# Performance work log

Measured on AMD Instinct MI355X. Metric: run time of the kernel, lower is better.

The kernel has to match this reference:

```python
import jax, jax.numpy as jnp
import numpy as np

N_PER, B, D, CIN, COUT = 500000, 2, 192, 64, 64
EPS = 1e-5


def _build_coords_and_nbrs():
    rng = np.random.default_rng(0)
    cells, xs, ys, zs = [], [], [], []
    for b in range(B):
        cell = rng.choice(D ** 3, size=N_PER, replace=False).astype(np.int64)
        cells.append(cell + b * D ** 3)
        xs.append(cell // (D * D))
        ys.append((cell // D) % D)
        zs.append(cell % D)
    lin = np.concatenate(cells)
    x = np.concatenate(xs); y = np.concatenate(ys); z = np.concatenate(zs)
    N = lin.shape[0]
    order = np.argsort(lin)
    slin = lin[order]

    def nbrs(axis_stride, cvals):
        cols = []
        for d in (-1, 0, 1):
            tgt = lin + d * axis_stride
            valid = (cvals + d >= 0) & (cvals + d < D)
            pos = np.searchsorted(slin, tgt)
            pc = np.clip(pos, 0, N - 1)
            found = valid & (slin[pc] == tgt)
            cols.append(np.where(found, order[pc], -1))
        return np.stack(cols, axis=1).astype(np.int32)  # [N,3]

    return nbrs(1, z), nbrs(D, y), nbrs(D * D, x)


def setup_inputs() -> dict:
    key = jax.random.key(0)
    k1, k2, k3, k4 = jax.random.split(key, 4)
    nbr_z, nbr_y, nbr_x = _build_coords_and_nbrs()
    N = B * N_PER
    s = 1.0 / np.sqrt(3.0 * CIN)
    return {
        "feats": jax.random.normal(k1, (N, CIN), jnp.float32),
        "W1": jax.random.normal(k2, (3, CIN, CIN), jnp.float32) * s,
        "W2": jax.random.normal(k3, (3, CIN, CIN), jnp.float32) * s,
        "W3": jax.random.normal(k4, (3, CIN, COUT), jnp.float32) * s,
        "gamma": jnp.ones((COUT,), jnp.float32),
        "beta": jnp.zeros((COUT,), jnp.float32),
        "nbr_z": jnp.asarray(nbr_z),
        "nbr_y": jnp.asarray(nbr_y),
        "nbr_x": jnp.asarray(nbr_x),
    }


def _sparse_conv1d(feats, W, nbr):
    # feats [N,Cin], W [3,Cin,Cout], nbr [N,3] (-1 = missing neighbor)
    mask = (nbr >= 0)
    g = feats[jnp.where(mask, nbr, 0)]              # [N,3,Cin] gather
    g = g * mask[..., None].astype(feats.dtype)     # zero missing taps
    return jnp.einsum('nkc,kcd->nd', g, W)          # GEMM over taps


def reference(feats, W1, W2, W3, gamma, beta, nbr_z, nbr_y, nbr_x):
    h = _sparse_conv1d(feats, W1, nbr_z)   # conv (1,1,3)
    h = _sparse_conv1d(h, W2, nbr_y)       # conv (1,3,1)
    h = _sparse_conv1d(h, W3, nbr_x)       # conv (3,1,1)
    # BatchNorm over the N active points (training-mode batch stats)
    mean = jnp.mean(h, axis=0)
    var = jnp.var(h, axis=0)
    h = (h - mean) * (gamma / jnp.sqrt(var + EPS)) + beta
    return jax.nn.relu(h)
```

## Files before the change

### kernel.cpp

```cpp
#include <hip/hip_runtime.h>
#include <cstdint>
#include <cstddef>


typedef __attribute__((ext_vector_type(4))) float float4v;
typedef __attribute__((ext_vector_type(4))) unsigned int uint4v;
typedef __attribute__((ext_vector_type(8))) __bf16 bf16x8;
typedef __attribute__((ext_vector_type(8))) unsigned short ushort8;

__device__ __forceinline__ unsigned short f2bf_bits(float f) {
    unsigned int u = __builtin_bit_cast(unsigned int, f);
    u += 0x7fffu + ((u >> 16) & 1u);
    return (unsigned short)(u >> 16);
}
__device__ __forceinline__ float bf2f(unsigned short b) {
    unsigned int u = ((unsigned int)b) << 16;
    return __builtin_bit_cast(float, u);
}

__device__ __forceinline__ void gld_lds16(const void* g, void* l) {
    __builtin_amdgcn_global_load_lds(
        (const __attribute__((address_space(1))) unsigned int*)g,
        (__attribute__((address_space(3))) unsigned int*)l, 16, 0, 0);
}

__global__ __launch_bounds__(256)
void cvt_kernel(const float* __restrict__ in, unsigned short* __restrict__ out,
                size_t n8)
{
    size_t i = (size_t)blockIdx.x * 256 + threadIdx.x;
    const size_t stride = (size_t)gridDim.x * 256;
    for (; i < n8; i += stride) {
        const float4v* p = reinterpret_cast<const float4v*>(in + i * 8);
        float4v f0 = p[0], f1 = p[1];
        ushort8 u;
#pragma unroll
        for (int j = 0; j < 4; ++j) {
            u[j]     = f2bf_bits(f0[j]);
            u[j + 4] = f2bf_bits(f1[j]);
        }
        *reinterpret_cast<uint4v*>(out + i * 8) = __builtin_bit_cast(uint4v, u);
    }
}

template<bool DO_STATS>
__global__ __launch_bounds__(256, 3)
void conv_kernel(const unsigned short* __restrict__ Ain,
                 const float* __restrict__ Wg,
                 const int* __restrict__ nbr,
                 unsigned short* __restrict__ Hout,
                 const unsigned short* __restrict__ Zrow,
                 float* __restrict__ stats, int ntiles)
{
    __shared__ unsigned short Bld[192 * 64];
    __shared__ unsigned short Abuf[4][2][1024];
    __shared__ unsigned short Tld[4][16 * 72];
    __shared__ float ssum[64], ssq[64];

    const int tid = threadIdx.x;
    for (int i = tid; i < 192 * 64; i += 256) {
        int kc = i >> 6, d = i & 63;
        Bld[(((kc >> 3) << 6) + d) * 8 + (kc & 7)] = f2bf_bits(Wg[i]);
    }
    if (DO_STATS && tid < 64) { ssum[tid] = 0.f; ssq[tid] = 0.f; }
    __syncthreads();

    const int lane = tid & 63;
    const int wid  = tid >> 6;
    const int l15  = lane & 15;
    const int quad = lane >> 4;

    bf16x8 bfr[6][4];
#pragma unroll
    for (int s = 0; s < 6; ++s)
#pragma unroll
        for (int nt = 0; nt < 4; ++nt) {
            const uint4v* p = reinterpret_cast<const uint4v*>(
                &Bld[(((s * 4 + quad) << 6) + nt * 16 + l15) * 8]);
            bfr[s][nt] = __builtin_bit_cast(bf16x8, *p);
        }

    const int rl  = lane >> 3;
    const int seg = (lane & 7) ^ rl;
    const char* zaddr = (const char*)Zrow + seg * 16;
    const char* abase = (const char*)Ain;

    const int frb = ((l15 >> 3) << 10) + ((l15 & 7) << 7);
    const int fr0 = frb + ((quad ^ (l15 & 7)) << 4);
    const int fr1 = frb + (((quad + 4) ^ (l15 & 7)) << 4);

    char* buf0 = (char*)&Abuf[wid][0][0];
    char* buf1 = (char*)&Abuf[wid][1][0];

    float lsum[4] = {0.f, 0.f, 0.f, 0.f};
    float lsq[4]  = {0.f, 0.f, 0.f, 0.f};
    unsigned short* tl = Tld[wid];

    const int S = gridDim.x * 4;
    int t = blockIdx.x * 4 + wid;
    if (t < ntiles) {
        int idxc[6], idxn[6];
#pragma unroll
        for (int tap = 0; tap < 3; ++tap)
#pragma unroll
            for (int h = 0; h < 2; ++h)
                idxc[tap * 2 + h] = nbr[(size_t)(t * 16 + h * 8 + rl) * 3 + tap];
        {
            int i0 = idxc[0], i1 = idxc[1];
            const char* g0 = (i0 >= 0) ? abase + (((size_t)(unsigned)i0) << 7) + seg * 16 : zaddr;
            const char* g1 = (i1 >= 0) ? abase + (((size_t)(unsigned)i1) << 7) + seg * 16 : zaddr;
            gld_lds16(g0, buf0);
            gld_lds16(g1, buf0 + 1024);
        }
        int tn = t + S;
        if (tn < ntiles) {
#pragma unroll
            for (int tap = 0; tap < 3; ++tap)
#pragma unroll
                for (int h = 0; h < 2; ++h)
                    idxn[tap * 2 + h] = nbr[(size_t)(tn * 16 + h * 8 + rl) * 3 + tap];
        }
        int p = 0;
        while (true) {
            float4v acc[4] = {};
#pragma unroll
            for (int tap = 0; tap < 3; ++tap) {
                char* curb = p ? buf1 : buf0;
                char* nxtb = p ? buf0 : buf1;
                __asm__ volatile("s_waitcnt vmcnt(0)" ::: "memory");
                uint4v ua0 = *reinterpret_cast<const uint4v*>(curb + fr0);
                uint4v ua1 = *reinterpret_cast<const uint4v*>(curb + fr1);
                int nj0, nj1;
                bool have_next;
                if (tap < 2) {
                    nj0 = idxc[(tap + 1) * 2]; nj1 = idxc[(tap + 1) * 2 + 1];
                    have_next = true;
                } else {
                    nj0 = idxn[0]; nj1 = idxn[1];
                    have_next = (tn < ntiles);
                }
                if (have_next) {
                    const char* g0 = (nj0 >= 0) ? abase + (((size_t)(unsigned)nj0) << 7) + seg * 16 : zaddr;
                    const char* g1 = (nj1 >= 0) ? abase + (((size_t)(unsigned)nj1) << 7) + seg * 16 : zaddr;
                    gld_lds16(g0, nxtb);
                    gld_lds16(g1, nxtb + 1024);
                }
                bf16x8 a0 = __builtin_bit_cast(bf16x8, ua0);
                bf16x8 a1 = __builtin_bit_cast(bf16x8, ua1);
                const int s0 = tap * 2;
#pragma unroll
                for (int nt = 0; nt < 4; ++nt)
                    acc[nt] = __builtin_amdgcn_mfma_f32_16x16x32_bf16(a0, bfr[s0][nt], acc[nt], 0, 0, 0);
#pragma unroll
                for (int nt = 0; nt < 4; ++nt)
                    acc[nt] = __builtin_amdgcn_mfma_f32_16x16x32_bf16(a1, bfr[s0 + 1][nt], acc[nt], 0, 0, 0);
                p ^= 1;
            }

            if (DO_STATS) {
#pragma unroll
                for (int nt = 0; nt < 4; ++nt) {
                    lsum[nt] += acc[nt][0] + acc[nt][1] + acc[nt][2] + acc[nt][3];
                    lsq[nt]  += acc[nt][0] * acc[nt][0] + acc[nt][1] * acc[nt][1]
                              + acc[nt][2] * acc[nt][2] + acc[nt][3] * acc[nt][3];
                }
            }

#pragma unroll
            for (int nt = 0; nt < 4; ++nt)
#pragma unroll
                for (int r = 0; r < 4; ++r)
                    tl[(quad * 4 + r) * 72 + nt * 16 + l15] = f2bf_bits(acc[nt][r]);
            __asm__ volatile("s_waitcnt lgkmcnt(0)" ::: "memory");
            unsigned short* op = Hout + ((size_t)t << 10);
#pragma unroll
            for (int c = 0; c < 2; ++c) {
                int chunk = c * 64 + lane;
                int r = chunk >> 3;
                int off = (chunk & 7) * 8;
                uint4v v = *reinterpret_cast<const uint4v*>(&tl[r * 72 + off]);
                *reinterpret_cast<uint4v*>(op + (r << 6) + off) = v;
            }
            __asm__ volatile("s_waitcnt lgkmcnt(0)" ::: "memory");

            t = tn; tn += S;
            if (t >= ntiles) break;
#pragma unroll
            for (int j = 0; j < 6; ++j) idxc[j] = idxn[j];
            if (tn < ntiles) {
#pragma unroll
                for (int tap = 0; tap < 3; ++tap)
#pragma unroll
                    for (int h = 0; h < 2; ++h)
                        idxn[tap * 2 + h] = nbr[(size_t)(tn * 16 + h * 8 + rl) * 3 + tap];
            }
        }
    }

    if (DO_STATS) {
#pragma unroll
        for (int nt = 0; nt < 4; ++nt) {
            atomicAdd(&ssum[nt * 16 + l15], lsum[nt]);
            atomicAdd(&ssq[nt * 16 + l15], lsq[nt]);
        }
        __syncthreads();
        if (tid < 64)               atomicAdd(&stats[tid], ssum[tid]);
        else if (tid < 128)         atomicAdd(&stats[tid], ssq[tid - 64]);
    }
}

__global__ __launch_bounds__(256)
void bn_relu_kernel(const unsigned short* __restrict__ H,
                    const float* __restrict__ stats,
                    const float* __restrict__ gamma,
                    const float* __restrict__ beta,
                    float* __restrict__ out, size_t ntot, float invN)
{
    __shared__ float sscale[64], sbias[64];
    const int tid = threadIdx.x;
    if (tid < 64) {
        float mean = stats[tid] * invN;
        float var  = stats[tid + 64] * invN - mean * mean;
        float sc   = gamma[tid] * rsqrtf(var + 1e-5f);
        sscale[tid] = sc;
        sbias[tid]  = beta[tid] - mean * sc;
    }
    __syncthreads();
    size_t i0 = ((size_t)blockIdx.x * 256 + tid) * 8;
    const size_t stride = (size_t)gridDim.x * 2048;
    const int cb = (int)(i0 & 63);
    float sc[8], bs[8];
#pragma unroll
    for (int j = 0; j < 8; ++j) { sc[j] = sscale[cb + j]; bs[j] = sbias[cb + j]; }
    for (size_t i = i0; i < ntot; i += stride) {
        uint4v v = *reinterpret_cast<const uint4v*>(H + i);
        float4v o0, o1;
#pragma unroll
        for (int j = 0; j < 4; ++j) {
            float lo = bf2f((unsigned short)(v[j] & 0xffffu));
            float hi = bf2f((unsigned short)(v[j] >> 16));
            float r0 = fmaxf(lo * sc[2 * j]     + bs[2 * j],     0.f);
            float r1 = fmaxf(hi * sc[2 * j + 1] + bs[2 * j + 1], 0.f);
            if (j < 2) { o0[2 * j] = r0; o0[2 * j + 1] = r1; }
            else       { o1[2 * (j - 2)] = r0; o1[2 * (j - 2) + 1] = r1; }
        }
        *reinterpret_cast<float4v*>(out + i)     = o0;
        *reinterpret_cast<float4v*>(out + i + 4) = o1;
    }
}

extern "C" void kernel_launch(void* const* d_in, const int* in_sizes, int n_in,
                              void* d_out, int out_size, void* d_ws, size_t ws_size,
                              hipStream_t stream)
{
    const float* feats = (const float*)d_in[0];
    const float* W1    = (const float*)d_in[1];
    const float* W2    = (const float*)d_in[2];
    const float* W3    = (const float*)d_in[3];
    const float* gamma = (const float*)d_in[4];
    const float* beta  = (const float*)d_in[5];
    const int* nbr_z   = (const int*)d_in[6];
    const int* nbr_y   = (const int*)d_in[7];
    const int* nbr_x   = (const int*)d_in[8];

    const int N = in_sizes[0] / 64;
    const int ntiles = N / 16;

    char* ws = (char*)d_ws;
    float* stats = (float*)ws;
    unsigned short* zrow = (unsigned short*)(ws + 512);
    unsigned short* a0 = (unsigned short*)(ws + 1024);
    unsigned short* h1 = a0 + (size_t)N * 64;
    unsigned short* h2 = h1 + (size_t)N * 64;
    unsigned short* h3 = a0;

    hipMemsetAsync(ws, 0, 1024, stream);

    dim3 blk(256);
    cvt_kernel<<<dim3(4096), blk, 0, stream>>>(feats, a0, (size_t)N * 8);
    conv_kernel<false><<<dim3(768), blk, 0, stream>>>(a0, W1, nbr_z, h1, zrow, nullptr, ntiles);
    conv_kernel<false><<<dim3(768), blk, 0, stream>>>(h1, W2, nbr_y, h2, zrow, nullptr, ntiles);
    conv_kernel<true ><<<dim3(768), blk, 0, stream>>>(h2, W3, nbr_x, h3, zrow, stats, ntiles);
    bn_relu_kernel<<<dim3(8192), blk, 0, stream>>>(h3, stats, gamma, beta,
                                                   (float*)d_out, (size_t)N * 64,
                                                   1.0f / (float)N);
}
```

Baseline: 756.0 us.

## Gather A fragments directly into registers and stream weights from LDS

The async global-to-LDS staging of gathered neighbor rows is replaced by direct per-lane global loads into registers, double-buffered across tiles with a two-tile software pipeline. The center tap reads the tile's own rows instead of the nbr index. Weights now stay in a fragment-ordered LDS layout and are read per MFMA instead of being held in registers, which frees VGPRs and allows occupancy 4 and a larger grid. The trade is more LDS read traffic per tile and exposed global latency, since prefetch depth is only one tile.

After: 708.9 us. 6.2% less time.

```diff
diff --git a/kernel.cpp b/kernel.cpp
--- a/kernel.cpp
+++ b/kernel.cpp
@@ -16,12 +16,6 @@
 __device__ __forceinline__ float bf2f(unsigned short b) {
     unsigned int u = ((unsigned int)b) << 16;
     return __builtin_bit_cast(float, u);
-}
-
-__device__ __forceinline__ void gld_lds16(const void* g, void* l) {
-    __builtin_amdgcn_global_load_lds(
-        (const __attribute__((address_space(1))) unsigned int*)g,
-        (__attribute__((address_space(3))) unsigned int*)l, 16, 0, 0);
 }
 
 __global__ __launch_bounds__(256)
@@ -43,8 +37,70 @@
     }
 }
 
+__device__ __forceinline__ void issue_tile(
+    uint4v (&A)[6], const char* __restrict__ abase,
+    const char* __restrict__ zaddr, int i0, int i2,
+    int t, int l15, int quad)
+{
+    const int qo = quad * 16;
+    const char* g0 = (i0 >= 0) ? abase + (((size_t)(unsigned)i0) << 7) : zaddr;
+    const char* gs = abase + (((size_t)(unsigned)(t * 16 + l15)) << 7);
+    const char* g2 = (i2 >= 0) ? abase + (((size_t)(unsigned)i2) << 7) : zaddr;
+    A[0] = *reinterpret_cast<const uint4v*>(g0 + qo);
+    A[1] = *reinterpret_cast<const uint4v*>(g0 + qo + 64);
+    A[2] = *reinterpret_cast<const uint4v*>(gs + qo);
+    A[3] = *reinterpret_cast<const uint4v*>(gs + qo + 64);
+    A[4] = *reinterpret_cast<const uint4v*>(g2 + qo);
+    A[5] = *reinterpret_cast<const uint4v*>(g2 + qo + 64);
+}
+
 template<bool DO_STATS>
-__global__ __launch_bounds__(256, 3)
+__device__ __forceinline__ void conv_tile(
+    const uint4v (&A)[6], const unsigned short* __restrict__ Bld,
+    unsigned short* __restrict__ tl, unsigned short* __restrict__ Hout,
+    int t, int lane, int l15, int quad,
+    float (&lsum)[4], float (&lsq)[4])
+{
+    float4v acc[4] = {};
+#pragma unroll
+    for (int s = 0; s < 6; ++s) {
+        bf16x8 a = __builtin_bit_cast(bf16x8, A[s]);
+#pragma unroll
+        for (int nt = 0; nt < 4; ++nt) {
+            uint4v ub = *reinterpret_cast<const uint4v*>(
+                Bld + (((s * 4 + nt) * 64 + lane) << 3));
+            bf16x8 b = __builtin_bit_cast(bf16x8, ub);
+            acc[nt] = __builtin_amdgcn_mfma_f32_16x16x32_bf16(a, b, acc[nt], 0, 0, 0);
+        }
+    }
+    if (DO_STATS) {
+#pragma unroll
+        for (int nt = 0; nt < 4; ++nt) {
+            lsum[nt] += acc[nt][0] + acc[nt][1] + acc[nt][2] + acc[nt][3];
+            lsq[nt]  += acc[nt][0] * acc[nt][0] + acc[nt][1] * acc[nt][1]
+                      + acc[nt][2] * acc[nt][2] + acc[nt][3] * acc[nt][3];
+        }
+    }
+#pragma unroll
+    for (int nt = 0; nt < 4; ++nt)
+#pragma unroll
+        for (int r = 0; r < 4; ++r)
+            tl[(quad * 4 + r) * 72 + nt * 16 + l15] = f2bf_bits(acc[nt][r]);
+    __asm__ volatile("s_waitcnt lgkmcnt(0)" ::: "memory");
+    unsigned short* op = Hout + ((size_t)t << 10);
+#pragma unroll
+    for (int c = 0; c < 2; ++c) {
+        int chunk = c * 64 + lane;
+        int r = chunk >> 3;
+        int off = (chunk & 7) * 8;
+        uint4v v = *reinterpret_cast<const uint4v*>(&tl[r * 72 + off]);
+        *reinterpret_cast<uint4v*>(op + (r << 6) + off) = v;
+    }
+    __asm__ volatile("s_waitcnt lgkmcnt(0)" ::: "memory");
+}
+
+template<bool DO_STATS>
+__global__ __launch_bounds__(256, 4)
 void conv_kernel(const unsigned short* __restrict__ Ain,
                  const float* __restrict__ Wg,
                  const int* __restrict__ nbr,
@@ -52,15 +108,18 @@
                  const unsigned short* __restrict__ Zrow,
                  float* __restrict__ stats, int ntiles)
 {
-    __shared__ unsigned short Bld[192 * 64];
-    __shared__ unsigned short Abuf[4][2][1024];
+    __shared__ unsigned short Bld[24 * 64 * 8];
     __shared__ unsigned short Tld[4][16 * 72];
     __shared__ float ssum[64], ssq[64];
 
     const int tid = threadIdx.x;
     for (int i = tid; i < 192 * 64; i += 256) {
         int kc = i >> 6, d = i & 63;
-        Bld[(((kc >> 3) << 6) + d) * 8 + (kc & 7)] = f2bf_bits(Wg[i]);
+        int tap = kc >> 6, c = kc & 63;
+        int s  = tap * 2 + (c >> 5);
+        int qd = (c >> 3) & 3, j = c & 7;
+        int ln = qd * 16 + (d & 15);
+        Bld[(((s * 4 + (d >> 4)) * 64 + ln) << 3) + j] = f2bf_bits(Wg[i]);
     }
     if (DO_STATS && tid < 64) { ssum[tid] = 0.f; ssq[tid] = 0.f; }
     __syncthreads();
@@ -69,131 +128,48 @@
     const int wid  = tid >> 6;
     const int l15  = lane & 15;
     const int quad = lane >> 4;
-
-    bf16x8 bfr[6][4];
-#pragma unroll
-    for (int s = 0; s < 6; ++s)
-#pragma unroll
-        for (int nt = 0; nt < 4; ++nt) {
-            const uint4v* p = reinterpret_cast<const uint4v*>(
-                &Bld[(((s * 4 + quad) << 6) + nt * 16 + l15) * 8]);
-            bfr[s][nt] = __builtin_bit_cast(bf16x8, *p);
-        }
-
-    const int rl  = lane >> 3;
-    const int seg = (lane & 7) ^ rl;
-    const char* zaddr = (const char*)Zrow + seg * 16;
     const char* abase = (const char*)Ain;
-
-    const int frb = ((l15 >> 3) << 10) + ((l15 & 7) << 7);
-    const int fr0 = frb + ((quad ^ (l15 & 7)) << 4);
-    const int fr1 = frb + (((quad + 4) ^ (l15 & 7)) << 4);
-
-    char* buf0 = (char*)&Abuf[wid][0][0];
-    char* buf1 = (char*)&Abuf[wid][1][0];
+    const char* zaddr = (const char*)Zrow;
+    unsigned short* tl = Tld[wid];
 
     float lsum[4] = {0.f, 0.f, 0.f, 0.f};
     float lsq[4]  = {0.f, 0.f, 0.f, 0.f};
-    unsigned short* tl = Tld[wid];
 
     const int S = gridDim.x * 4;
     int t = blockIdx.x * 4 + wid;
     if (t < ntiles) {
-        int idxc[6], idxn[6];
-#pragma unroll
-        for (int tap = 0; tap < 3; ++tap)
-#pragma unroll
-            for (int h = 0; h < 2; ++h)
-                idxc[tap * 2 + h] = nbr[(size_t)(t * 16 + h * 8 + rl) * 3 + tap];
-        {
-            int i0 = idxc[0], i1 = idxc[1];
-            const char* g0 = (i0 >= 0) ? abase + (((size_t)(unsigned)i0) << 7) + seg * 16 : zaddr;
-            const char* g1 = (i1 >= 0) ? abase + (((size_t)(unsigned)i1) << 7) + seg * 16 : zaddr;
-            gld_lds16(g0, buf0);
-            gld_lds16(g1, buf0 + 1024);
-        }
+        size_t nb = (size_t)(t * 16 + l15) * 3;
+        int iA0 = nbr[nb], iA2 = nbr[nb + 2];
+        int iB0 = 0, iB2 = 0;
+        uint4v Aa[6], Ab[6];
+        issue_tile(Aa, abase, zaddr, iA0, iA2, t, l15, quad);
         int tn = t + S;
         if (tn < ntiles) {
-#pragma unroll
-            for (int tap = 0; tap < 3; ++tap)
-#pragma unroll
-                for (int h = 0; h < 2; ++h)
-                    idxn[tap * 2 + h] = nbr[(size_t)(tn * 16 + h * 8 + rl) * 3 + tap];
-        }
-        int p = 0;
+            size_t nb1 = (size_t)(tn * 16 + l15) * 3;
+            iA0 = nbr[nb1]; iA2 = nbr[nb1 + 2];
+        }
         while (true) {
-            float4v acc[4] = {};
-#pragma unroll
-            for (int tap = 0; tap < 3; ++tap) {
-                char* curb = p ? buf1 : buf0;
-                char* nxtb = p ? buf0 : buf1;
-                __asm__ volatile("s_waitcnt vmcnt(0)" ::: "memory");
-                uint4v ua0 = *reinterpret_cast<const uint4v*>(curb + fr0);
-                uint4v ua1 = *reinterpret_cast<const uint4v*>(curb + fr1);
-                int nj0, nj1;
-                bool have_next;
-                if (tap < 2) {
-                    nj0 = idxc[(tap + 1) * 2]; nj1 = idxc[(tap + 1) * 2 + 1];
-                    have_next = true;
-                } else {
-                    nj0 = idxn[0]; nj1 = idxn[1];
-                    have_next = (tn < ntiles);
-                }
-                if (have_next) {
-                    const char* g0 = (nj0 >= 0) ? abase + (((size_t)(unsigned)nj0) << 7) + seg * 16 : zaddr;
-                    const char* g1 = (nj1 >= 0) ? abase + (((size_t)(unsigned)nj1) << 7) + seg * 16 : zaddr;
-                    gld_lds16(g0, nxtb);
-                    gld_lds16(g1, nxtb + 1024);
-                }
-                bf16x8 a0 = __builtin_bit_cast(bf16x8, ua0);
-                bf16x8 a1 = __builtin_bit_cast(bf16x8, ua1);
-                const int s0 = tap * 2;
-#pragma unroll
-                for (int nt = 0; nt < 4; ++nt)
-                    acc[nt] = __builtin_amdgcn_mfma_f32_16x16x32_bf16(a0, bfr[s0][nt], acc[nt], 0, 0, 0);
-#pragma unroll
-                for (int nt = 0; nt < 4; ++nt)
-                    acc[nt] = __builtin_amdgcn_mfma_f32_16x16x32_bf16(a1, bfr[s0 + 1][nt], acc[nt], 0, 0, 0);
-                p ^= 1;
+            int t2 = tn + S;
+            if (t2 < ntiles) {
+                size_t nb2 = (size_t)(t2 * 16 + l15) * 3;
+                iB0 = nbr[nb2]; iB2 = nbr[nb2 + 2];
             }
-
-            if (DO_STATS) {
-#pragma unroll
-                for (int nt = 0; nt < 4; ++nt) {
-                    lsum[nt] += acc[nt][0] + acc[nt][1] + acc[nt][2] + acc[nt][3];
-                    lsq[nt]  += acc[nt][0] * acc[nt][0] + acc[nt][1] * acc[nt][1]
-                              + acc[nt][2] * acc[nt][2] + acc[nt][3] * acc[nt][3];
-                }
+            if (tn < ntiles)
+                issue_tile(Ab, abase, zaddr, iA0, iA2, tn, l15, quad);
+            conv_tile<DO_STATS>(Aa, Bld, tl, Hout, t, lane, l15, quad, lsum, lsq);
+            t = tn; tn = t2;
+            if (t >= ntiles) break;
+
+            t2 = tn + S;
+            if (t2 < ntiles) {
+                size_t nb2 = (size_t)(t2 * 16 + l15) * 3;
+                iA0 = nbr[nb2]; iA2 = nbr[nb2 + 2];
             }
-
-#pragma unroll
-            for (int nt = 0; nt < 4; ++nt)
-#pragma unroll
-                for (int r = 0; r < 4; ++r)
-                    tl[(quad * 4 + r) * 72 + nt * 16 + l15] = f2bf_bits(acc[nt][r]);
-            __asm__ volatile("s_waitcnt lgkmcnt(0)" ::: "memory");
-            unsigned short* op = Hout + ((size_t)t << 10);
-#pragma unroll
-            for (int c = 0; c < 2; ++c) {
-                int chunk = c * 64 + lane;
-                int r = chunk >> 3;
-                int off = (chunk & 7) * 8;
-                uint4v v = *reinterpret_cast<const uint4v*>(&tl[r * 72 + off]);
-                *reinterpret_cast<uint4v*>(op + (r << 6) + off) = v;
-            }
-            __asm__ volatile("s_waitcnt lgkmcnt(0)" ::: "memory");
-
-            t = tn; tn += S;
+            if (tn < ntiles)
+                issue_tile(Aa, abase, zaddr, iB0, iB2, tn, l15, quad);
+            conv_tile<DO_STATS>(Ab, Bld, tl, Hout, t, lane, l15, quad, lsum, lsq);
+            t = tn; tn = t2;
             if (t >= ntiles) break;
-#pragma unroll
-            for (int j = 0; j < 6; ++j) idxc[j] = idxn[j];
-            if (tn < ntiles) {
-#pragma unroll
-                for (int tap = 0; tap < 3; ++tap)
-#pragma unroll
-                    for (int h = 0; h < 2; ++h)
-                        idxn[tap * 2 + h] = nbr[(size_t)(tn * 16 + h * 8 + rl) * 3 + tap];
-            }
         }
     }
 
@@ -278,9 +254,9 @@
 
     dim3 blk(256);
     cvt_kernel<<<dim3(4096), blk, 0, stream>>>(feats, a0, (size_t)N * 8);
-    conv_kernel<false><<<dim3(768), blk, 0, stream>>>(a0, W1, nbr_z, h1, zrow, nullptr, ntiles);
-    conv_kernel<false><<<dim3(768), blk, 0, stream>>>(h1, W2, nbr_y, h2, zrow, nullptr, ntiles);
-    conv_kernel<true ><<<dim3(768), blk, 0, stream>>>(h2, W3, nbr_x, h3, zrow, stats, ntiles);
+    conv_kernel<false><<<dim3(1024), blk, 0, stream>>>(a0, W1, nbr_z, h1, zrow, nullptr, ntiles);
+    conv_kernel<false><<<dim3(1024), blk, 0, stream>>>(h1, W2, nbr_y, h2, zrow, nullptr, ntiles);
+    conv_kernel<true ><<<dim3(1024), blk, 0, stream>>>(h2, W3, nbr_x, h3, zrow, stats, ntiles);
     bn_relu_kernel<<<dim3(8192), blk, 0, stream>>>(h3, stats, gamma, beta,
                                                    (float*)d_out, (size_t)N * 64,
                                                    1.0f / (float)N);
```
